# Performance work log

Measured on AMD Instinct MI355X. Metric: run time of the kernel, lower is better.

Reference implementation:

```python
import jax, jax.numpy as jnp
import numpy as np
import math

FACTOR = 5  # self.factor


def setup_inputs() -> dict:
    key = jax.random.key(0)
    kq, kk, kv, ki = jax.random.split(key, 4)
    B, L_Q, L_K, H, D = 16, 4096, 4096, 8, 64
    sample_k = min(FACTOR * math.ceil(math.log(L_K)), L_K)  # U_part = 45
    queries = jax.random.normal(kq, (B, L_Q, H, D), jnp.float32)
    keys = jax.random.normal(kk, (B, L_K, H, D), jnp.float32)
    values = jax.random.normal(kv, (B, L_K, H, D), jnp.float32)
    # replicates torch.randint(L_K, (L_Q, sample_k)) in _prob_QK
    index_sample = jax.random.randint(ki, (L_Q, sample_k), 0, L_K, dtype=jnp.int32)
    return {"queries": queries, "keys": keys, "values": values,
            "index_sample": index_sample}


def reference(queries, keys, values, index_sample):
    B, L_Q, H, D = queries.shape
    L_K = keys.shape[1]
    # transpose to [B, H, L, D] as in forward
    Q = jnp.transpose(queries, (0, 2, 1, 3))
    K = jnparrays = None
    K = jnp.transpose(keys, (0, 2, 1, 3))
    V = jnp.transpose(values, (0, 2, 1, 3))

    n_top = min(FACTOR * math.ceil(math.log(L_Q)), L_Q)  # u = 45

    # --- _prob_QK: sampled score estimate ---
    # K_sample[b,h,q,s,:] = K[b,h,index_sample[q,s],:]
    K_sample = K[:, :, index_sample, :]                      # [B,H,L_Q,sk,D]
    QK_sample = jnp.einsum('bhqd,bhqsd->bhqs', Q, K_sample)  # [B,H,L_Q,sk]
    M = QK_sample.max(axis=-1) - QK_sample.sum(axis=-1) / L_K
    M_top = jax.lax.top_k(M, n_top)[1]                       # [B,H,u]

    Q_reduce = jnp.take_along_axis(Q, M_top[..., None], axis=2)  # [B,H,u,D]
    scores = jnp.einsum('bhud,bhkd->bhuk', Q_reduce, K)          # [B,H,u,L_K]
    scale = 1.0 / math.sqrt(D)  # self.scale is None -> 1/sqrt(D)
    scores = scores * scale

    # --- initial context: mean of V broadcast over L_Q ---
    context = jnp.broadcast_to(V.mean(axis=2, keepdims=True), (B, H, L_Q, D))

    # --- update context at selected query positions ---
    attn = jax.nn.softmax(scores, axis=-1)
    ctx_top = jnp.einsum('bhuk,bhkd->bhud', attn, V)             # [B,H,u,D]
    bi = jnp.arange(B)[:, None, None]
    hi = jnp.arange(H)[None, :, None]
    context = context.at[bi, hi, M_top].set(ctx_top)

    return jnp.transpose(context, (0, 2, 1, 3))  # [B,L_Q,H,D]
```

## Files before the change

kernel.cpp:

```cpp
#include <hip/hip_runtime.h>
#include <hip/hip_bf16.h>
#include <math.h>

#define B_ 16
#define L_ 4096
#define H_ 8
#define D_ 64
#define S_ 45
#define U_ 45
#define BH_ (B_*H_)
#define NC_ 8
#define CK_ (L_/NC_)

#define OFF_MEAN 0
#define OFF_MP   (OFF_MEAN + BH_*D_)
#define OFF_M    (OFF_MP + 16*BH_*D_)
#define OFF_TOPQ (OFF_M + BH_*L_)
#define OFF_PL   (OFF_TOPQ + BH_*U_ + 32)
#define OFF_PCTX (OFF_PL + BH_*NC_*U_)

__global__ void mean_kernel(const float* __restrict__ V, float* __restrict__ mp) {
    int bid = blockIdx.x;
    int bh = bid >> 4, chunk = bid & 15;
    int b = bh >> 3, h = bh & 7;
    int t = threadIdx.x;
    int d = t & 63, r0 = t >> 6;
    float sum = 0.f;
    int base = ((b*L_ + chunk*256)*H_ + h)*D_ + d;
    for (int r = r0; r < 256; r += 4)
        sum += V[base + r*(H_*D_)];
    __shared__ float sm[256];
    sm[t] = sum; __syncthreads();
    if (t < 64) {
        float s = sm[t] + sm[t+64] + sm[t+128] + sm[t+192];
        mp[chunk*(BH_*D_) + bh*D_ + t] = s;
    }
}

__global__ void meanfin_kernel(const float* __restrict__ mp, float* __restrict__ mean) {
    int i = blockIdx.x*256 + threadIdx.x;
    float s = 0.f;
    for (int c = 0; c < 16; ++c) s += mp[c*(BH_*D_) + i];
    mean[i] = s * (1.0f/L_);
}

__global__ void fill_kernel(const float* __restrict__ mean, float4* __restrict__ out4) {
    int total = B_*L_*H_*D_/4;
    for (int i = blockIdx.x*blockDim.x + threadIdx.x; i < total; i += gridDim.x*blockDim.x) {
        int e = i << 2;
        int d = e & 63;
        int h = (e >> 6) & 7;
        int b = e >> 21;
        out4[i] = *(const float4*)&mean[((b<<3)+h)*D_ + d];
    }
}

__device__ __forceinline__ float dpp_add16(float x) {
    int xi, yi;
    xi = __float_as_int(x);
    yi = __builtin_amdgcn_update_dpp(0, xi, 0xB1, 0xf, 0xf, true);
    x += __int_as_float(yi);
    xi = __float_as_int(x);
    yi = __builtin_amdgcn_update_dpp(0, xi, 0x4E, 0xf, 0xf, true);
    x += __int_as_float(yi);
    xi = __float_as_int(x);
    yi = __builtin_amdgcn_update_dpp(0, xi, 0x141, 0xf, 0xf, true);
    x += __int_as_float(yi);
    xi = __float_as_int(x);
    yi = __builtin_amdgcn_update_dpp(0, xi, 0x140, 0xf, 0xf, true);
    x += __int_as_float(yi);
    return x;
}

__global__ __launch_bounds__(256) void m_kernel(const float* __restrict__ Q,
                                                const float* __restrict__ K,
                                                const int* __restrict__ idx,
                                                float* __restrict__ M) {
    int bid = blockIdx.x;
    int xcd  = bid & 7;
    int slot = bid >> 3;
    int q0 = slot*32;
    int t = threadIdx.x;
    int wave = t >> 6, lane = t & 63;

    __shared__ int silds[32*48];
    for (int g = t; g < 32*48; g += 256) {
        int u = g / 48, s = g - u*48;
        if (s < S_) silds[g] = idx[(q0+u)*S_ + s];
    }
    __syncthreads();

    int grp = lane >> 4;
    int d4 = (lane & 15) * 4;
    int myq = wave*4 + grp;

    for (int si = 0; si < 16; ++si) {
        int slab = xcd*16 + si;
        int b = slab >> 3, h = slab & 7;
        const float* Kb = K + b*(L_*H_*D_) + h*D_;
        for (int half = 0; half < 2; ++half) {
            int qq = myq + half*16;
            int q = q0 + qq;
            const int* myidx = &silds[qq*48];
            float4 q4 = *(const float4*)&Q[(b*L_ + q)*(H_*D_) + h*D_ + d4];
            float maxv = -3.0e38f, sumv = 0.f;
            #pragma unroll 2
            for (int c = 0; c < 11; ++c) {
                int4 k4 = *(const int4*)&myidx[c*4];
                {
                    float4 kv = *(const float4*)&Kb[k4.x*(H_*D_) + d4];
                    float p = q4.x*kv.x + q4.y*kv.y + q4.z*kv.z + q4.w*kv.w;
                    p = dpp_add16(p); maxv = fmaxf(maxv, p); sumv += p;
                }
                {
                    float4 kv = *(const float4*)&Kb[k4.y*(H_*D_) + d4];
                    float p = q4.x*kv.x + q4.y*kv.y + q4.z*kv.z + q4.w*kv.w;
                    p = dpp_add16(p); maxv = fmaxf(maxv, p); sumv += p;
                }
                {
                    float4 kv = *(const float4*)&Kb[k4.z*(H_*D_) + d4];
                    float p = q4.x*kv.x + q4.y*kv.y + q4.z*kv.z + q4.w*kv.w;
                    p = dpp_add16(p); maxv = fmaxf(maxv, p); sumv += p;
                }
                {
                    float4 kv = *(const float4*)&Kb[k4.w*(H_*D_) + d4];
                    float p = q4.x*kv.x + q4.y*kv.y + q4.z*kv.z + q4.w*kv.w;
                    p = dpp_add16(p); maxv = fmaxf(maxv, p); sumv += p;
                }
            }
            {
                int k = myidx[44];
                float4 kv = *(const float4*)&Kb[k*(H_*D_) + d4];
                float p = q4.x*kv.x + q4.y*kv.y + q4.z*kv.z + q4.w*kv.w;
                p = dpp_add16(p); maxv = fmaxf(maxv, p); sumv += p;
            }
            if ((lane & 15) == 0)
                M[slab*L_ + q] = maxv - sumv * (1.0f/L_);
        }
    }
}

__global__ __launch_bounds__(256) void topk_kernel(const float* __restrict__ M,
                                                   int* __restrict__ topq) {
    int wave = threadIdx.x >> 6, lane = threadIdx.x & 63;
    int bh = blockIdx.x*4 + wave;
    const float* Mr = M + bh*L_;
    float v[64];
    #pragma unroll
    for (int j = 0; j < 64; ++j) v[j] = Mr[j*64 + lane];
    for (int it = 0; it < U_; ++it) {
        float lm = v[0]; int lj = 0;
        #pragma unroll
        for (int j = 1; j < 64; ++j) {
            bool g = v[j] > lm;
            lm = g ? v[j] : lm;
            lj = g ? j : lj;
        }
        float bm = lm; int bi = lj*64 + lane;
        #pragma unroll
        for (int off = 1; off < 64; off <<= 1) {
            float om = __shfl_xor(bm, off);
            int   oi = __shfl_xor(bi, off);
            if (om > bm || (om == bm && oi < bi)) { bm = om; bi = oi; }
        }
        if (lane == 0) topq[bh*U_ + it] = bi;
        int wl = bi & 63, wj = bi >> 6;
        if (lane == wl) {
            #pragma unroll
            for (int j = 0; j < 64; ++j)
                if (j == wj) v[j] = -3.0e38f;
        }
    }
}

__global__ __launch_bounds__(256, 2) void attn_kernel(
        const float* __restrict__ Q, const float* __restrict__ K, const float* __restrict__ V,
        const int* __restrict__ topq,
        float* __restrict__ pl, float* __restrict__ pctx) {
    int bid = blockIdx.x;
    int bh = bid / NC_, c = bid % NC_;
    int b = bh >> 3, h = bh & 7;
    int t = threadIdx.x, wave = t >> 6, lane = t & 63;

    __shared__ int   qidx_s[U_];
    __shared__ float klds[64*64];
    __shared__ float wlds[48*64];

    if (t < U_) qidx_s[t] = topq[bh*U_ + t];
    __syncthreads();

    float lpart[12], ctx_u[12];
    #pragma unroll
    for (int j = 0; j < 12; ++j) { lpart[j] = 0.f; ctx_u[j] = 0.f; }

    int k0base = c*CK_;
    for (int sc = 0; sc < CK_/64; ++sc) {
        int k0 = k0base + sc*64;
        __syncthreads();
        for (int g = t; g < 64*16; g += 256) {
            int r = g >> 4, cc = g & 15;
            const float4* kr = (const float4*)&K[((b*L_ + k0 + r)*H_ + h)*D_];
            ((float4*)klds)[r*16 + (cc ^ (r & 15))] = kr[cc];
        }
        __syncthreads();

        float dotu[12];
        #pragma unroll
        for (int j = 0; j < 12; ++j) dotu[j] = 0.f;
        #pragma unroll
        for (int dh = 0; dh < 2; ++dh) {
            float4 kreg[8];
            #pragma unroll
            for (int cc = 0; cc < 8; ++cc)
                kreg[cc] = ((float4*)klds)[lane*16 + ((dh*8 + cc) ^ (lane & 15))];
            #pragma unroll
            for (int j = 0; j < 12; ++j) {
                int u = wave + 4*j;
                if (u >= U_) break;
                int qrow = __builtin_amdgcn_readfirstlane(qidx_s[u]);
                const float* qp = Q + ((size_t)(b*L_ + qrow)*H_ + h)*D_ + dh*32;
                float d0 = 0.f, d1 = 0.f, d2 = 0.f, d3 = 0.f;
                #pragma unroll
                for (int cc = 0; cc < 8; ++cc) {
                    float4 kv = kreg[cc];
                    d0 += qp[cc*4+0]*kv.x; d1 += qp[cc*4+1]*kv.y;
                    d2 += qp[cc*4+2]*kv.z; d3 += qp[cc*4+3]*kv.w;
                }
                dotu[j] += (d0+d1)+(d2+d3);
            }
        }
        #pragma unroll
        for (int j = 0; j < 12; ++j) {
            int u = wave + 4*j;
            if (u >= U_) break;
            float e = __expf(dotu[j] * 0.125f);
            lpart[j] += e;
            wlds[u*64 + lane] = e;
        }

        float vreg[64];
        #pragma unroll
        for (int jj = 0; jj < 64; ++jj)
            vreg[jj] = V[((b*L_ + k0 + jj)*H_ + h)*D_ + lane];
        #pragma unroll
        for (int j = 0; j < 12; ++j) {
            int u = wave + 4*j;
            if (u >= U_) break;
            float a0 = 0.f, a1 = 0.f, a2 = 0.f, a3 = 0.f;
            const float4* w4 = (const float4*)&wlds[u*64];
            #pragma unroll
            for (int cc = 0; cc < 16; ++cc) {
                float4 wv = w4[cc];
                a0 += wv.x*vreg[cc*4];   a1 += wv.y*vreg[cc*4+1];
                a2 += wv.z*vreg[cc*4+2]; a3 += wv.w*vreg[cc*4+3];
            }
            ctx_u[j] += (a0+a1)+(a2+a3);
        }
    }

    #pragma unroll
    for (int j = 0; j < 12; ++j) {
        int u = wave + 4*j;
        if (u >= U_) break;
        float l = lpart[j];
        #pragma unroll
        for (int o = 32; o; o >>= 1) l += __shfl_xor(l, o);
        int pbase = (bh*NC_ + c)*U_ + u;
        if (lane == 0) pl[pbase] = l;
        pctx[pbase*D_ + lane] = ctx_u[j];
    }
}

__global__ void combine_kernel(const float* __restrict__ pl,
                               const float* __restrict__ pctx, const int* __restrict__ topq,
                               float* __restrict__ out) {
    int bh = blockIdx.x; int b = bh >> 3, h = bh & 7;
    int t = threadIdx.x;
    int lane_d = t & 63, usub = t >> 6;
    for (int u = usub; u < U_; u += 4) {
        int pb = bh*NC_*U_ + u;
        float lg = 0.f, cx = 0.f;
        for (int cc = 0; cc < NC_; ++cc) {
            lg += pl[pb + cc*U_];
            cx += pctx[(pb + cc*U_)*D_ + lane_d];
        }
        int q = topq[bh*U_ + u];
        out[((b*L_ + q)*H_ + h)*D_ + lane_d] = cx / lg;
    }
}

extern "C" void kernel_launch(void* const* d_in, const int* in_sizes, int n_in,
                              void* d_out, int out_size, void* d_ws, size_t ws_size,
                              hipStream_t stream) {
    const float* Q  = (const float*)d_in[0];
    const float* K  = (const float*)d_in[1];
    const float* V  = (const float*)d_in[2];
    const int* idx  = (const int*)d_in[3];
    float* out = (float*)d_out;
    float* ws  = (float*)d_ws;

    float* mean = ws + OFF_MEAN;
    float* mp   = ws + OFF_MP;
    float* M    = ws + OFF_M;
    int*   topq = (int*)(ws + OFF_TOPQ);
    float* pl   = ws + OFF_PL;
    float* pctx = ws + OFF_PCTX;

    mean_kernel   <<<BH_*16, 256, 0, stream>>>(V, mp);
    meanfin_kernel<<<(BH_*D_)/256, 256, 0, stream>>>(mp, mean);
    fill_kernel   <<<2048, 256, 0, stream>>>(mean, (float4*)out);
    m_kernel      <<<1024, 256, 0, stream>>>(Q, K, idx, M);
    topk_kernel   <<<BH_/4, 256, 0, stream>>>(M, topq);
    attn_kernel   <<<BH_*NC_, 256, 0, stream>>>(Q, K, V, topq, pl, pctx);
    combine_kernel<<<BH_, 256, 0, stream>>>(pl, pctx, topq, out);
}
```

Measured before the change: 746.3 us.

## Software-pipeline sampled K gathers and load K rows directly in attention

```diff
diff --git a/kernel.cpp b/kernel.cpp
--- a/kernel.cpp
+++ b/kernel.cpp
@@ -72,6 +72,9 @@
     return x;
 }
 
+#define MRED(kv) { float p_ = q4.x*(kv).x + q4.y*(kv).y + q4.z*(kv).z + q4.w*(kv).w; \
+                   p_ = dpp_add16(p_); maxv = fmaxf(maxv, p_); sumv += p_; }
+
 __global__ __launch_bounds__(256) void m_kernel(const float* __restrict__ Q,
                                                 const float* __restrict__ K,
                                                 const int* __restrict__ idx,
@@ -104,35 +107,31 @@
             const int* myidx = &silds[qq*48];
             float4 q4 = *(const float4*)&Q[(b*L_ + q)*(H_*D_) + h*D_ + d4];
             float maxv = -3.0e38f, sumv = 0.f;
-            #pragma unroll 2
-            for (int c = 0; c < 11; ++c) {
-                int4 k4 = *(const int4*)&myidx[c*4];
-                {
-                    float4 kv = *(const float4*)&Kb[k4.x*(H_*D_) + d4];
-                    float p = q4.x*kv.x + q4.y*kv.y + q4.z*kv.z + q4.w*kv.w;
-                    p = dpp_add16(p); maxv = fmaxf(maxv, p); sumv += p;
-                }
-                {
-                    float4 kv = *(const float4*)&Kb[k4.y*(H_*D_) + d4];
-                    float p = q4.x*kv.x + q4.y*kv.y + q4.z*kv.z + q4.w*kv.w;
-                    p = dpp_add16(p); maxv = fmaxf(maxv, p); sumv += p;
-                }
-                {
-                    float4 kv = *(const float4*)&Kb[k4.z*(H_*D_) + d4];
-                    float p = q4.x*kv.x + q4.y*kv.y + q4.z*kv.z + q4.w*kv.w;
-                    p = dpp_add16(p); maxv = fmaxf(maxv, p); sumv += p;
-                }
-                {
-                    float4 kv = *(const float4*)&Kb[k4.w*(H_*D_) + d4];
-                    float p = q4.x*kv.x + q4.y*kv.y + q4.z*kv.z + q4.w*kv.w;
-                    p = dpp_add16(p); maxv = fmaxf(maxv, p); sumv += p;
-                }
+            int4 ka = *(const int4*)&myidx[0];
+            float4 f0 = *(const float4*)&Kb[ka.x*(H_*D_) + d4];
+            float4 f1 = *(const float4*)&Kb[ka.y*(H_*D_) + d4];
+            float4 f2 = *(const float4*)&Kb[ka.z*(H_*D_) + d4];
+            float4 f3 = *(const float4*)&Kb[ka.w*(H_*D_) + d4];
+            #pragma unroll
+            for (int c2 = 0; c2 < 5; ++c2) {
+                int4 kb_ = *(const int4*)&myidx[(2*c2+1)*4];
+                float4 g0 = *(const float4*)&Kb[kb_.x*(H_*D_) + d4];
+                float4 g1 = *(const float4*)&Kb[kb_.y*(H_*D_) + d4];
+                float4 g2 = *(const float4*)&Kb[kb_.z*(H_*D_) + d4];
+                float4 g3 = *(const float4*)&Kb[kb_.w*(H_*D_) + d4];
+                MRED(f0); MRED(f1); MRED(f2); MRED(f3);
+                int4 kc = *(const int4*)&myidx[(2*c2+2)*4];
+                f0 = *(const float4*)&Kb[kc.x*(H_*D_) + d4];
+                f1 = *(const float4*)&Kb[kc.y*(H_*D_) + d4];
+                f2 = *(const float4*)&Kb[kc.z*(H_*D_) + d4];
+                f3 = *(const float4*)&Kb[kc.w*(H_*D_) + d4];
+                MRED(g0); MRED(g1); MRED(g2); MRED(g3);
             }
+            MRED(f0); MRED(f1); MRED(f2); MRED(f3);
             {
                 int k = myidx[44];
                 float4 kv = *(const float4*)&Kb[k*(H_*D_) + d4];
-                float p = q4.x*kv.x + q4.y*kv.y + q4.z*kv.z + q4.w*kv.w;
-                p = dpp_add16(p); maxv = fmaxf(maxv, p); sumv += p;
+                MRED(kv);
             }
             if ((lane & 15) == 0)
                 M[slab*L_ + q] = maxv - sumv * (1.0f/L_);
@@ -183,7 +182,6 @@
     int t = threadIdx.x, wave = t >> 6, lane = t & 63;
 
     __shared__ int   qidx_s[U_];
-    __shared__ float klds[64*64];
     __shared__ float wlds[48*64];
 
     if (t < U_) qidx_s[t] = topq[bh*U_ + t];
@@ -196,13 +194,7 @@
     int k0base = c*CK_;
     for (int sc = 0; sc < CK_/64; ++sc) {
         int k0 = k0base + sc*64;
-        __syncthreads();
-        for (int g = t; g < 64*16; g += 256) {
-            int r = g >> 4, cc = g & 15;
-            const float4* kr = (const float4*)&K[((b*L_ + k0 + r)*H_ + h)*D_];
-            ((float4*)klds)[r*16 + (cc ^ (r & 15))] = kr[cc];
-        }
-        __syncthreads();
+        const float* Krow = K + ((size_t)(b*L_ + k0 + lane)*H_ + h)*D_;
 
         float dotu[12];
         #pragma unroll
@@ -212,7 +204,7 @@
             float4 kreg[8];
             #pragma unroll
             for (int cc = 0; cc < 8; ++cc)
-                kreg[cc] = ((float4*)klds)[lane*16 + ((dh*8 + cc) ^ (lane & 15))];
+                kreg[cc] = *(const float4*)&Krow[dh*32 + cc*4];
             #pragma unroll
             for (int j = 0; j < 12; ++j) {
                 int u = wave + 4*j;
```

Result: faster. 664.8 us, median of 2 (-10.9%).
